# Kernel optimization log

Hardware: AMD Instinct MI355X
Metric: run time of the kernel (lower is better)

Reference implementation:

```python
import jax, jax.numpy as jnp
import numpy as np

B, T, D, DU, H = 2048, 100, 128, 128, 128  # batch, seq_len, emb_dim, user_emb_dim, hidden (=emb_dim)


def _mlp(x, layers, act):
    for W, b in layers:
        x = act(x @ W.T + b)
    return x


def setup_inputs() -> dict:
    key = jax.random.key(0)
    ks = iter(jax.random.split(key, 48))
    def p(shape, scale=0.05):
        return jax.random.normal(next(ks), shape, jnp.float32) * scale
    lengths = jax.random.randint(next(ks), (B,), 1, T + 1).astype(jnp.int32)
    mask = (jnp.arange(T)[None, :] < lengths[:, None]).astype(jnp.int32)
    inp = {
        'user_embedding': p((B, DU), 1.0),
        'item_historical_embedding': p((B, T, D), 1.0),
        'item_embedding': p((B, D), 1.0),
        'mask': mask,
        'sequential_length': lengths,
        'gru_Wih': p((3 * H, D)), 'gru_Whh': p((3 * H, H)),
        'gru_bih': p((3 * H,)), 'gru_bhh': p((3 * H,)),
        'aug_Wr': p((H, D + H)), 'aug_br': p((H,)),
        'aug_Wu': p((H, D + H)), 'aug_bu': p((H,)),
        'aug_Wh': p((H, D + H)), 'aug_bh': p((H,)),
    }
    att_dims = [4 * D, 80, 40, 1]
    ph_dims = [4 * D + DU, 200, 80, 1]
    for i, (di, do) in enumerate(zip(att_dims[:-1], att_dims[1:])):
        inp['att_W%d' % i] = p((do, di)); inp['att_b%d' % i] = p((do,))
    for i, (di, do) in enumerate(zip(ph_dims[:-1], ph_dims[1:])):
        inp['ph_W%d' % i] = p((do, di)); inp['ph_b%d' % i] = p((do,))
    return inp


def _forward(mask, sequential_length, user_embedding, item_historical_embedding, item_embedding,
             gru_Wih, gru_Whh, gru_bih, gru_bhh,
             att_W0, att_b0, att_W1, att_b1, att_W2, att_b2,
             aug_Wr, aug_br, aug_Wu, aug_bu, aug_Wh, aug_bh,
             ph_W0, ph_b0, ph_W1, ph_b1, ph_W2, ph_b2):
    fmask = mask.astype(jnp.float32)
    hist_sum = (item_historical_embedding * fmask[:, :, None]).sum(1)
    hist_sum = hist_sum / sequential_length[:, None].astype(jnp.float32)  # (B, D)

    # standard GRU over time (torch nn.GRU gate math) via lax.scan
    def gru_step(h, x_t):
        gi = x_t @ gru_Wih.T + gru_bih
        gh = h @ gru_Whh.T + gru_bhh
        i_r, i_z, i_n = jnp.split(gi, 3, axis=-1)
        h_r, h_z, h_n = jnp.split(gh, 3, axis=-1)
        r = jax.nn.sigmoid(i_r + h_r)
        z = jax.nn.sigmoid(i_z + h_z)
        n = jnp.tanh(i_n + r * h_n)
        h_new = (1.0 - z) * n + z * h
        return h_new, h_new
    h0 = jnp.zeros((item_historical_embedding.shape[0], H), jnp.float32)
    _, gru_seq = jax.lax.scan(gru_step, h0, jnp.swapaxes(item_historical_embedding, 0, 1))
    keys = jnp.swapaxes(gru_seq, 0, 1)  # (B, T, H)

    # DIN-style activation unit (all-ReLU MLP since act='relu'), masked softmax over time
    q = jnp.broadcast_to(item_embedding[:, None, :], keys.shape)
    feat = jnp.concatenate([keys, q, keys - q, q * keys], axis=-1)  # (B, T, 4H)
    score = _mlp(feat, [(att_W0, att_b0), (att_W1, att_b1), (att_W2, att_b2)], jax.nn.relu)
    score = jnp.where(mask[:, :, None] == 1, score, -jnp.inf)
    attn = jax.nn.softmax(score, axis=1)[..., 0]  # (B, T)
    # return_score=False in source: pooled context vector is (mis)used as attention scores
    pooled = jnp.einsum('bt,btd->bd', attn, keys)  # (B, H)

    # AUGRU; source indexes pooled[:, t] as per-step attention score (requires T <= H)
    att_seq = pooled.T[:T]  # (T, B)
    def augru_step(h, inp):
        x_t, a_t = inp
        ti = jnp.concatenate([h, x_t], axis=-1)
        r = jax.nn.sigmoid(ti @ aug_Wr.T + aug_br)
        u = jax.nn.sigmoid(ti @ aug_Wu.T + aug_bu)
        h_hat = jnp.tanh(jnp.concatenate([h * r, x_t], axis=-1) @ aug_Wh.T + aug_bh)
        u = a_t[:, None] * u
        h_new = (1.0 - u) * h + u * h_hat
        return h_new, h_new
    _, aug_seq = jax.lax.scan(augru_step, h0, (jnp.swapaxes(keys, 0, 1), att_seq))
    aug_out = jnp.swapaxes(aug_seq, 0, 1)  # (B, T, H)

    idx = (sequential_length - 1).astype(jnp.int32)[:, None, None]
    attention_feature = jnp.take_along_axis(aug_out, idx, axis=1)[:, 0, :]  # (B, H)

    comb = jnp.concatenate([user_embedding, item_embedding, hist_sum,
                            item_embedding * hist_sum, attention_feature], axis=1)
    # PredictHead: all layers sigmoid (source's i != len(dims)-1 is always True)
    scores = _mlp(comb, [(ph_W0, ph_b0), (ph_W1, ph_b1), (ph_W2, ph_b2)], jax.nn.sigmoid)
    return scores[:, 0]


def reference(user_embedding, item_historical_embedding, item_embedding, mask, sequential_length,
              gru_Wih, gru_Whh, gru_bih, gru_bhh,
              att_W0, att_b0, att_W1, att_b1, att_W2, att_b2,
              aug_Wr, aug_br, aug_Wu, aug_bu, aug_Wh, aug_bh,
              ph_W0, ph_b0, ph_W1, ph_b1, ph_W2, ph_b2):
    return _forward(mask, sequential_length, user_embedding, item_historical_embedding, item_embedding,
                    gru_Wih, gru_Whh, gru_bih, gru_bhh,
                    att_W0, att_b0, att_W1, att_b1, att_W2, att_b2,
                    aug_Wr, aug_br, aug_Wu, aug_bu, aug_Wh, aug_bh,
                    ph_W0, ph_b0, ph_W1, ph_b1, ph_W2, ph_b2)
```

## Files before the change

kernel.cpp:

```cpp
#include <hip/hip_runtime.h>
#include <math.h>

#define BB 2048
#define TT 100
#define DD 128
#define HH 128

typedef __attribute__((ext_vector_type(8))) short bf16x8;
typedef __attribute__((ext_vector_type(4))) float f32x4;

__device__ __forceinline__ float sigm(float x) {
    return __builtin_amdgcn_rcpf(1.f + __expf(-x));
}
__device__ __forceinline__ float tanh_fast(float x) {
    x = fminf(fmaxf(x, -15.f), 15.f);
    float e = __expf(2.f * x);
    return (e - 1.f) * __builtin_amdgcn_rcpf(e + 1.f);
}
__device__ __forceinline__ short f2bf(float f) {
    union { float f; unsigned u; } v; v.f = f;
    unsigned r = v.u + 0x7FFF + ((v.u >> 16) & 1);
    return (short)(r >> 16);
}
__device__ __forceinline__ float bf2f(ushort u) {
    union { unsigned u; float f; } v; v.u = ((unsigned)u) << 16;
    return v.f;
}

#define RD_A(buf, kk) (*(const bf16x8*)((const char*)(buf) + arow * 256 + (((kk) * 64 + akg * 16) ^ ((arow & 7) << 4))))
#define ST_A(buf, row, c, val) (*(short*)((char*)(buf) + (row) * 256 + (((c) * 2) ^ (((row) & 7) << 4))) = (val))

__global__ void k_prep(const float* __restrict__ attW0,
                       float* __restrict__ Wk, float* __restrict__ Wd, float* __restrict__ WqmC) {
    int i = blockIdx.x * 256 + threadIdx.x;
    if (i < 128 * 80) {
        int d = i / 80, j = i - d * 80;
        Wk[i]   = attW0[j * 512 + d] + attW0[j * 512 + 256 + d];
        Wd[i]   = attW0[j * 512 + 384 + d];
        WqmC[i] = attW0[j * 512 + 128 + d] - attW0[j * 512 + 256 + d];
    }
}

__global__ void k_pack(const float* __restrict__ Wih, const float* __restrict__ Whh,
                       const float* __restrict__ Wr, const float* __restrict__ Wu, const float* __restrict__ Wh,
                       const float* __restrict__ attW1,
                       const float* __restrict__ phW0, const float* __restrict__ phW1,
                       ushort* __restrict__ Pgru, ushort* __restrict__ Pa1, ushort* __restrict__ Pa2,
                       ushort* __restrict__ W1bf, ushort* __restrict__ W0h, ushort* __restrict__ W1h) {
    int n = blockIdx.x * 256 + threadIdx.x;
    if (n < 98304) {
        int tile = n >> 11, kt = (n >> 9) & 3, li = (n >> 3) & 63, e = n & 7;
        int k = kt * 32 + (li >> 4) * 8 + e;
        float s;
        if (tile < 24) { int j = tile * 16 + (li & 15); s = Wih[j * 128 + k]; }
        else           { int j = (tile - 24) * 16 + (li & 15); s = Whh[j * 128 + k]; }
        Pgru[n] = (ushort)f2bf(s);
    }
    if (n < 65536) {
        int tile = n >> 12, kt = (n >> 9) & 7, li = (n >> 3) & 63, e = n & 7;
        int k = kt * 32 + (li >> 4) * 8 + e;
        int jj = tile * 16 + (li & 15);
        float s = (jj < 128) ? Wr[jj * 256 + k] : Wu[(jj - 128) * 256 + k];
        Pa1[n] = (ushort)f2bf(s);
    }
    if (n < 32768) {
        int tile = n >> 12, kt = (n >> 9) & 7, li = (n >> 3) & 63, e = n & 7;
        int k = kt * 32 + (li >> 4) * 8 + e;
        int j = tile * 16 + (li & 15);
        Pa2[n] = (ushort)f2bf(Wh[j * 256 + k]);
    }
    if (n < 4608) {
        int g = n >> 9;
        int nt = g / 3, kt = g - nt * 3;
        int li = (n >> 3) & 63, e = n & 7;
        int k = kt * 32 + (li >> 4) * 8 + e;
        int j2 = nt * 16 + (li & 15);
        float s = (k < 80 && j2 < 40) ? attW1[j2 * 80 + k] : 0.f;
        W1bf[n] = (ushort)f2bf(s);
    }
    if (n < 133120) {
        int g = n >> 9;
        int nt = g / 20, kt = g - nt * 20;
        int li = (n >> 3) & 63, e = n & 7;
        int k = kt * 32 + (li >> 4) * 8 + e;
        int j = nt * 16 + (li & 15);
        W0h[n] = (ushort)f2bf((j < 200) ? phW0[j * 640 + k] : 0.f);
    }
    if (n < 17920) {
        int g = n >> 9;
        int nt = g / 7, kt = g - nt * 7;
        int li = (n >> 3) & 63, e = n & 7;
        int k = kt * 32 + (li >> 4) * 8 + e;
        int j = nt * 16 + (li & 15);
        W1h[n] = (ushort)f2bf((k < 200 && j < 80) ? phW1[j * 200 + k] : 0.f);
    }
}

__global__ void k_weffbf(const float* __restrict__ item, const float* __restrict__ Wk,
                         const float* __restrict__ Wd, const float* __restrict__ WqmC,
                         const float* __restrict__ attb0,
                         ushort* __restrict__ Weffbf, float* __restrict__ bias2) {
    int b = blockIdx.x, tid = threadIdx.x;
    __shared__ float q[128];
    if (tid < 128) q[tid] = item[b * 128 + tid];
    __syncthreads();
    ushort* Wb = Weffbf + (size_t)b * 10240;
    for (int idx = tid; idx < 10240; idx += 256) {
        int e = idx & 7, li = (idx >> 3) & 63, kt = (idx >> 9) & 3, nt = idx >> 11;
        int d = kt * 32 + (li >> 4) * 8 + e;
        int j = nt * 16 + (li & 15);
        Wb[idx] = (ushort)f2bf(Wk[d * 80 + j] + q[d] * Wd[d * 80 + j]);
    }
    if (tid < 80) {
        float s = attb0[tid];
        for (int d = 0; d < 128; ++d) s += q[d] * WqmC[d * 80 + tid];
        bias2[b * 80 + tid] = s;
    }
}

__global__ __launch_bounds__(512) void k_gru_mfma(const float* __restrict__ hist,
                                                  const ushort* __restrict__ Wp,
                                                  const float* __restrict__ bih, const float* __restrict__ bhh,
                                                  const int* __restrict__ len,
                                                  ushort* __restrict__ keysbf, float* __restrict__ hsum) {
    int tid = threadIdx.x;
    int lane = tid & 63, w = tid >> 6;
    int b0 = blockIdx.x * 8;

    __shared__ ushort xbf[16 * 128];
    __shared__ ushort hbf[2][16 * 128];
    __shared__ int    ln_s[8];

    for (int e = tid; e < 16 * 128; e += 512) { xbf[e] = 0; hbf[0][e] = 0; hbf[1][e] = 0; }
    if (tid < 8) ln_s[tid] = len[b0 + tid];

    const bf16x8* Wv = (const bf16x8*)Wp;
    bf16x8 bfx[3][4], bfh[3][4];
#pragma unroll
    for (int g = 0; g < 3; ++g)
#pragma unroll
        for (int kt = 0; kt < 4; ++kt) {
            bfx[g][kt] = Wv[((g * 8 + w) * 4 + kt) * 64 + lane];
            bfh[g][kt] = Wv[(((24 + g * 8 + w)) * 4 + kt) * 64 + lane];
        }

    int arow = lane & 15, akg = lane >> 4;
    int c = w * 16 + arow;
    float birq = bih[c] + bhh[c];
    float bizq = bih[128 + c] + bhh[128 + c];
    float bin  = bih[256 + c];
    float bqn  = bhh[256 + c];
    float hold[4] = {0.f, 0.f, 0.f, 0.f};

    __syncthreads();

    int srow = tid >> 6, sd0 = (tid & 63) * 2;
    int Lrow = ln_s[srow];
    const float* hsrc = &hist[(size_t)(b0 + srow) * TT * DD + sd0];
    float2 v = *(const float2*)hsrc;
    float sum0 = 0.f, sum1 = 0.f;
    int p = 0;

    for (int t = 0; t < TT; ++t) {
        {
            unsigned pv = (unsigned)(unsigned short)f2bf(v.x) | ((unsigned)(unsigned short)f2bf(v.y) << 16);
            *(unsigned*)((char*)xbf + srow * 256 + ((sd0 * 2) ^ ((srow & 7) << 4))) = pv;
            if (t < Lrow) { sum0 += v.x; sum1 += v.y; }
            if (t + 1 < TT) v = *(const float2*)(hsrc + (size_t)(t + 1) * DD);
        }
        __syncthreads();

        const ushort* hb = hbf[p];
        bf16x8 ax[4], ah[4];
#pragma unroll
        for (int kt = 0; kt < 4; ++kt) { ax[kt] = RD_A(xbf, kt); ah[kt] = RD_A(hb, kt); }

        f32x4 accr = {0.f,0.f,0.f,0.f}, accz = {0.f,0.f,0.f,0.f};
        f32x4 accnx = {0.f,0.f,0.f,0.f}, accnh = {0.f,0.f,0.f,0.f};
#pragma unroll
        for (int kt = 0; kt < 4; ++kt) {
            accr  = __builtin_amdgcn_mfma_f32_16x16x32_bf16(ax[kt], bfx[0][kt], accr, 0, 0, 0);
            accr  = __builtin_amdgcn_mfma_f32_16x16x32_bf16(ah[kt], bfh[0][kt], accr, 0, 0, 0);
            accz  = __builtin_amdgcn_mfma_f32_16x16x32_bf16(ax[kt], bfx[1][kt], accz, 0, 0, 0);
            accz  = __builtin_amdgcn_mfma_f32_16x16x32_bf16(ah[kt], bfh[1][kt], accz, 0, 0, 0);
            accnx = __builtin_amdgcn_mfma_f32_16x16x32_bf16(ax[kt], bfx[2][kt], accnx, 0, 0, 0);
            accnh = __builtin_amdgcn_mfma_f32_16x16x32_bf16(ah[kt], bfh[2][kt], accnh, 0, 0, 0);
        }

        ushort* hbw = (ushort*)hbf[p ^ 1];
#pragma unroll
        for (int i = 0; i < 4; ++i) {
            float r = sigm(accr[i] + birq);
            float z = sigm(accz[i] + bizq);
            float nn = tanh_fast(accnx[i] + bin + r * (accnh[i] + bqn));
            float hnew = (1.f - z) * nn + z * hold[i];
            hold[i] = hnew;
            if (akg < 2) {
                int row = akg * 4 + i;
                short hb16 = f2bf(hnew);
                ST_A(hbw, row, c, hb16);
                keysbf[((size_t)(b0 + row) * TT + t) * HH + c] = (ushort)hb16;
            }
        }
        p ^= 1;
        __syncthreads();
    }

    hsum[(b0 + srow) * 128 + sd0]     = sum0 / (float)Lrow;
    hsum[(b0 + srow) * 128 + sd0 + 1] = sum1 / (float)Lrow;
}

__global__ __launch_bounds__(512) void k_attnsoft(const ushort* __restrict__ keysbf,
                                                  const ushort* __restrict__ Weffbf,
                                                  const float* __restrict__ bias2,
                                                  const ushort* __restrict__ W1bf,
                                                  const float* __restrict__ attb1, const float* __restrict__ attW2,
                                                  const float* __restrict__ attb2,
                                                  const int* __restrict__ len,
                                                  float* __restrict__ pooled) {
    int tid = threadIdx.x;
    int lane = tid & 63, w = tid >> 6;
    int b = blockIdx.x;

    __shared__ ushort kbf[112 * 128];
    __shared__ ushort scbf[112 * 96];
    __shared__ float  bias2s[80];
    __shared__ float  b1s[48];
    __shared__ float  W2s[48];
    __shared__ float  attn_s[128];
    __shared__ float  red[128];

    bf16x8 bfrag0[5][4];
    bf16x8 bfrag1[3][3];
    if (w < 7) {
        const bf16x8* Wb = (const bf16x8*)(Weffbf + (size_t)b * 10240);
#pragma unroll
        for (int nt = 0; nt < 5; ++nt)
#pragma unroll
            for (int kt = 0; kt < 4; ++kt)
                bfrag0[nt][kt] = Wb[(nt * 4 + kt) * 64 + lane];
#pragma unroll
        for (int nt = 0; nt < 3; ++nt)
#pragma unroll
            for (int kt = 0; kt < 3; ++kt)
                bfrag1[nt][kt] = ((const bf16x8*)W1bf)[(nt * 3 + kt) * 64 + lane];
    }

    const ushort* ksrc = keysbf + (size_t)b * TT * 128;
    for (int e = tid; e < 3584; e += 512) {
        int row = e >> 5, c4 = e & 31;
        uint2 pv;
        if (row < TT) pv = *(const uint2*)(ksrc + row * 128 + c4 * 4);
        else { pv.x = 0; pv.y = 0; }
        *(uint2*)((char*)kbf + row * 256 + ((c4 * 8) ^ ((row & 7) << 4))) = pv;
    }
    for (int e = tid; e < 1792; e += 512) {
        int row = e >> 4, c = 80 + (e & 15);
        *(ushort*)((char*)scbf + row * 192 + ((c * 2) ^ ((row & 7) << 4))) = 0;
    }
    if (tid < 80) bias2s[tid] = bias2[b * 80 + tid];
    if (tid < 48) {
        b1s[tid] = (tid < 40) ? attb1[tid] : 0.f;
        W2s[tid] = (tid < 40) ? attW2[tid] : 0.f;
    }
    __syncthreads();

    if (w < 7) {
        int arow = lane & 15, akg = lane >> 4;
        int row = w * 16 + arow;
        bf16x8 af[4];
#pragma unroll
        for (int kt = 0; kt < 4; ++kt)
            af[kt] = *(const bf16x8*)((const char*)kbf + row * 256 + (((kt * 64 + akg * 16)) ^ ((row & 7) << 4)));
#pragma unroll
        for (int nt = 0; nt < 5; ++nt) {
            f32x4 acc = {0.f, 0.f, 0.f, 0.f};
#pragma unroll
            for (int kt = 0; kt < 4; ++kt)
                acc = __builtin_amdgcn_mfma_f32_16x16x32_bf16(af[kt], bfrag0[nt][kt], acc, 0, 0, 0);
            int col = nt * 16 + arow;
            float bcol = bias2s[col];
#pragma unroll
            for (int i = 0; i < 4; ++i) {
                int r2 = w * 16 + akg * 4 + i;
                float vsc = fmaxf(acc[i] + bcol, 0.f);
                *(short*)((char*)scbf + r2 * 192 + ((col * 2) ^ ((r2 & 7) << 4))) = f2bf(vsc);
            }
        }
    }
    __syncthreads();

    if (w < 7) {
        int arow = lane & 15, akg = lane >> 4;
        int row = w * 16 + arow;
        bf16x8 a1[3];
#pragma unroll
        for (int kt = 0; kt < 3; ++kt)
            a1[kt] = *(const bf16x8*)((const char*)scbf + row * 192 + (((kt * 64 + akg * 16)) ^ ((row & 7) << 4)));
        float pi[4] = {0.f, 0.f, 0.f, 0.f};
#pragma unroll
        for (int nt = 0; nt < 3; ++nt) {
            f32x4 acc = {0.f, 0.f, 0.f, 0.f};
#pragma unroll
            for (int kt = 0; kt < 3; ++kt)
                acc = __builtin_amdgcn_mfma_f32_16x16x32_bf16(a1[kt], bfrag1[nt][kt], acc, 0, 0, 0);
            int col = nt * 16 + arow;
            float wb = W2s[col], bb1 = b1s[col];
#pragma unroll
            for (int i = 0; i < 4; ++i)
                pi[i] += fmaxf(acc[i] + bb1, 0.f) * wb;
        }
#pragma unroll
        for (int off = 1; off < 16; off <<= 1)
#pragma unroll
            for (int i = 0; i < 4; ++i)
                pi[i] += __shfl_xor(pi[i], off);
        if ((lane & 15) == 0) {
            float b2 = attb2[0];
#pragma unroll
            for (int i = 0; i < 4; ++i) {
                int t = w * 16 + akg * 4 + i;
                if (t < 128) attn_s[t] = fmaxf(pi[i] + b2, 0.f);
            }
        }
    }
    __syncthreads();

    int L = len[b];
    if (tid < 128) red[tid] = (tid < L) ? attn_s[tid] : -INFINITY;
    __syncthreads();
    for (int o = 64; o >= 1; o >>= 1) { if (tid < o) red[tid] = fmaxf(red[tid], red[tid + o]); __syncthreads(); }
    float mx = red[0];
    __syncthreads();
    if (tid < 128) {
        float e = (tid < L) ? __expf(attn_s[tid] - mx) : 0.f;
        attn_s[tid] = e; red[tid] = e;
    }
    __syncthreads();
    for (int o = 64; o >= 1; o >>= 1) { if (tid < o) red[tid] += red[tid + o]; __syncthreads(); }
    float inv = __builtin_amdgcn_rcpf(red[0]);
    if (tid < 128) {
        int d = tid;
        float p = 0.f;
        for (int t2 = 0; t2 < L; ++t2) {
            ushort kv = *(const ushort*)((const char*)kbf + t2 * 256 + ((d * 2) ^ ((t2 & 7) << 4)));
            p += attn_s[t2] * bf2f(kv);
        }
        pooled[b * 128 + d] = p * inv;
    }
}

__global__ __launch_bounds__(512) void k_augru_mfma(const ushort* __restrict__ keysbf,
                                                    const float* __restrict__ pooled,
                                                    const int* __restrict__ len,
                                                    const ushort* __restrict__ Wp1, const ushort* __restrict__ Wp2,
                                                    const float* __restrict__ br, const float* __restrict__ bu,
                                                    const float* __restrict__ bh,
                                                    float* __restrict__ att_feat) {
    int tid = threadIdx.x;
    int lane = tid & 63, w = tid >> 6;
    int b0 = blockIdx.x * 8;

    __shared__ ushort hbf[16 * 128], xbf[16 * 128], rhbf[16 * 128];
    __shared__ float as_[16];
    __shared__ int ln_s[8];

    for (int e = tid; e < 16 * 128; e += 512) { hbf[e] = 0; xbf[e] = 0; rhbf[e] = 0; }
    if (tid < 16) as_[tid] = 0.f;
    if (tid < 8) ln_s[tid] = len[b0 + tid];

    const bf16x8* W1v = (const bf16x8*)Wp1;
    const bf16x8* W2v = (const bf16x8*)Wp2;
    bf16x8 b1r[8], b1u[8], b2[8];
#pragma unroll
    for (int kt = 0; kt < 8; ++kt) {
        b1r[kt] = W1v[(w * 8 + kt) * 64 + lane];
        b1u[kt] = W1v[((8 + w) * 8 + kt) * 64 + lane];
        b2[kt]  = W2v[(w * 8 + kt) * 64 + lane];
    }

    int arow = lane & 15, akg = lane >> 4;
    int c = w * 16 + arow;
    float brc = br[c], buc = bu[c], bhc = bh[c];
    float hold[4] = {0.f, 0.f, 0.f, 0.f};

    int srow = tid >> 6, sd0 = (tid & 63) * 2;
    const ushort* xsrc = &keysbf[(size_t)(b0 + srow) * TT * HH + sd0];
    unsigned v0 = *(const unsigned*)xsrc;
    __syncthreads();
    *(unsigned*)((char*)xbf + srow * 256 + ((sd0 * 2) ^ ((srow & 7) << 4))) = v0;
    unsigned vnext = (TT > 1) ? *(const unsigned*)(xsrc + (size_t)1 * HH) : 0u;
    float areg = 0.f;
    if (tid < 8) {
        as_[tid] = pooled[(b0 + tid) * HH + 0];
        if (TT > 1) areg = pooled[(b0 + tid) * HH + 1];
    }
    __syncthreads();

    for (int t = 0; t < TT; ++t) {
        bf16x8 ah[4], ax[4];
#pragma unroll
        for (int kt = 0; kt < 4; ++kt) { ah[kt] = RD_A(hbf, kt); ax[kt] = RD_A(xbf, kt); }
        f32x4 accr = {0.f,0.f,0.f,0.f}, accu = {0.f,0.f,0.f,0.f};
#pragma unroll
        for (int kt = 0; kt < 4; ++kt) {
            accr = __builtin_amdgcn_mfma_f32_16x16x32_bf16(ah[kt], b1r[kt], accr, 0, 0, 0);
            accr = __builtin_amdgcn_mfma_f32_16x16x32_bf16(ax[kt], b1r[4 + kt], accr, 0, 0, 0);
            accu = __builtin_amdgcn_mfma_f32_16x16x32_bf16(ah[kt], b1u[kt], accu, 0, 0, 0);
            accu = __builtin_amdgcn_mfma_f32_16x16x32_bf16(ax[kt], b1u[4 + kt], accu, 0, 0, 0);
        }
        float u_reg[4];
#pragma unroll
        for (int i = 0; i < 4; ++i) {
            float r = sigm(accr[i] + brc);
            float a = as_[akg * 4 + i];
            u_reg[i] = a * sigm(accu[i] + buc);
            if (akg < 2) ST_A(rhbf, akg * 4 + i, c, f2bf(r * hold[i]));
        }
        __syncthreads();

        bf16x8 arh[4];
#pragma unroll
        for (int kt = 0; kt < 4; ++kt) arh[kt] = RD_A(rhbf, kt);
        f32x4 acch = {0.f,0.f,0.f,0.f};
#pragma unroll
        for (int kt = 0; kt < 4; ++kt) {
            acch = __builtin_amdgcn_mfma_f32_16x16x32_bf16(arh[kt], b2[kt], acch, 0, 0, 0);
            acch = __builtin_amdgcn_mfma_f32_16x16x32_bf16(ax[kt], b2[4 + kt], acch, 0, 0, 0);
        }
#pragma unroll
        for (int i = 0; i < 4; ++i) {
            float hhat = tanh_fast(acch[i] + bhc);
            float hnew = (1.f - u_reg[i]) * hold[i] + u_reg[i] * hhat;
            hold[i] = hnew;
            if (akg < 2) {
                int row = akg * 4 + i;
                ST_A(hbf, row, c, f2bf(hnew));
                if (t == ln_s[row] - 1) att_feat[(b0 + row) * HH + c] = hnew;
            }
        }
        if (t + 1 < TT) {
            *(unsigned*)((char*)xbf + srow * 256 + ((sd0 * 2) ^ ((srow & 7) << 4))) = vnext;
            if (tid < 8) as_[tid] = areg;
            if (t + 2 < TT) {
                vnext = *(const unsigned*)(xsrc + (size_t)(t + 2) * HH);
                if (tid < 8) areg = pooled[(b0 + tid) * HH + t + 2];
            }
        }
        __syncthreads();
    }
}

__global__ __launch_bounds__(64) void k_head(const float* __restrict__ user, const float* __restrict__ item,
                                             const float* __restrict__ hsum, const float* __restrict__ attf,
                                             const ushort* __restrict__ W0h, const ushort* __restrict__ W1h,
                                             const float* __restrict__ phb0, const float* __restrict__ phb1,
                                             const float* __restrict__ phW2, const float* __restrict__ phb2,
                                             float* __restrict__ out) {
    int lane = threadIdx.x;
    int b0 = blockIdx.x * 16;
    __shared__ ushort xb[16 * 128];
    __shared__ ushort h1b[16 * 256];

    for (int e = lane; e < 4096; e += 64) h1b[e] = 0;

    int arow = lane & 15, akg = lane >> 4;
    f32x4 acc0[13];
#pragma unroll
    for (int nt = 0; nt < 13; ++nt) acc0[nt] = (f32x4){0.f, 0.f, 0.f, 0.f};

    for (int c = 0; c < 5; ++c) {
        for (int idx = lane; idx < 1024; idx += 64) {
            int row = idx >> 6, c2 = (idx & 63) * 2;
            int g = (b0 + row) * 128 + c2;
            float2 v;
            if (c == 0) v = *(const float2*)&user[g];
            else if (c == 1) v = *(const float2*)&item[g];
            else if (c == 2) v = *(const float2*)&hsum[g];
            else if (c == 3) { float2 a = *(const float2*)&item[g]; float2 h = *(const float2*)&hsum[g];
                               v.x = a.x * h.x; v.y = a.y * h.y; }
            else v = *(const float2*)&attf[g];
            unsigned pv = (unsigned)(unsigned short)f2bf(v.x) | ((unsigned)(unsigned short)f2bf(v.y) << 16);
            *(unsigned*)((char*)xb + row * 256 + ((c2 * 2) ^ ((row & 7) << 4))) = pv;
        }
        __syncthreads();
        bf16x8 af[4];
#pragma unroll
        for (int kt = 0; kt < 4; ++kt)
            af[kt] = *(const bf16x8*)((const char*)xb + arow * 256 + ((kt * 64 + akg * 16) ^ ((arow & 7) << 4)));
#pragma unroll
        for (int nt = 0; nt < 13; ++nt) {
#pragma unroll
            for (int kt = 0; kt < 4; ++kt) {
                int ktg = c * 4 + kt;
                bf16x8 bf = ((const bf16x8*)W0h)[(nt * 20 + ktg) * 64 + lane];
                acc0[nt] = __builtin_amdgcn_mfma_f32_16x16x32_bf16(af[kt], bf, acc0[nt], 0, 0, 0);
            }
        }
        __syncthreads();
    }

#pragma unroll
    for (int nt = 0; nt < 13; ++nt) {
        int col = nt * 16 + arow;
        if (col < 200) {
            float bb = phb0[col];
#pragma unroll
            for (int i = 0; i < 4; ++i) {
                int r2 = akg * 4 + i;
                *(short*)((char*)h1b + r2 * 512 + ((col * 2) ^ ((r2 & 7) << 4))) = f2bf(sigm(acc0[nt][i] + bb));
            }
        }
    }
    __syncthreads();

    bf16x8 a1[7];
#pragma unroll
    for (int kt = 0; kt < 7; ++kt)
        a1[kt] = *(const bf16x8*)((const char*)h1b + arow * 512 + ((kt * 64 + akg * 16) ^ ((arow & 7) << 4)));
    float pi[4] = {0.f, 0.f, 0.f, 0.f};
#pragma unroll
    for (int nt = 0; nt < 5; ++nt) {
        f32x4 acc = {0.f, 0.f, 0.f, 0.f};
#pragma unroll
        for (int kt = 0; kt < 7; ++kt)
            acc = __builtin_amdgcn_mfma_f32_16x16x32_bf16(a1[kt], ((const bf16x8*)W1h)[(nt * 7 + kt) * 64 + lane], acc, 0, 0, 0);
        int col = nt * 16 + arow;
        float b1 = phb1[col], w2v = phW2[col];
#pragma unroll
        for (int i = 0; i < 4; ++i)
            pi[i] += sigm(acc[i] + b1) * w2v;
    }
#pragma unroll
    for (int off = 1; off < 16; off <<= 1)
#pragma unroll
        for (int i = 0; i < 4; ++i)
            pi[i] += __shfl_xor(pi[i], off);
    if (arow == 0) {
        float b2 = phb2[0];
#pragma unroll
        for (int i = 0; i < 4; ++i)
            out[b0 + akg * 4 + i] = sigm(pi[i] + b2);
    }
}

extern "C" void kernel_launch(void* const* d_in, const int* in_sizes, int n_in,
                              void* d_out, int out_size, void* d_ws, size_t ws_size,
                              hipStream_t stream) {
    const float* user = (const float*)d_in[0];
    const float* hist = (const float*)d_in[1];
    const float* item = (const float*)d_in[2];
    const int* len = (const int*)d_in[4];
    const float* gWih = (const float*)d_in[5];
    const float* gWhh = (const float*)d_in[6];
    const float* gbih = (const float*)d_in[7];
    const float* gbhh = (const float*)d_in[8];
    const float* aWr = (const float*)d_in[9];
    const float* abr = (const float*)d_in[10];
    const float* aWu = (const float*)d_in[11];
    const float* abu = (const float*)d_in[12];
    const float* aWh = (const float*)d_in[13];
    const float* abh = (const float*)d_in[14];
    const float* attW0 = (const float*)d_in[15];
    const float* attb0 = (const float*)d_in[16];
    const float* attW1 = (const float*)d_in[17];
    const float* attb1 = (const float*)d_in[18];
    const float* attW2 = (const float*)d_in[19];
    const float* attb2 = (const float*)d_in[20];
    const float* phW0 = (const float*)d_in[21];
    const float* phb0 = (const float*)d_in[22];
    const float* phW1 = (const float*)d_in[23];
    const float* phb1 = (const float*)d_in[24];
    const float* phW2 = (const float*)d_in[25];
    const float* phb2 = (const float*)d_in[26];

    char* ws = (char*)d_ws;
    size_t off = 0;
    auto alloc = [&](size_t bytes) { char* p = ws + off; off += (bytes + 255) & ~(size_t)255; return p; };
    ushort* keysbf  = (ushort*)alloc((size_t)BB * TT * HH * 2);
    ushort* Weffbf  = (ushort*)alloc((size_t)BB * 10240 * 2);
    float* pooled   = (float*)alloc((size_t)BB * HH * 4);
    float* hsum     = (float*)alloc((size_t)BB * DD * 4);
    float* attf     = (float*)alloc((size_t)BB * HH * 4);
    float* Wk       = (float*)alloc(128 * 80 * 4);
    float* Wd       = (float*)alloc(128 * 80 * 4);
    float* WqmC     = (float*)alloc(128 * 80 * 4);
    float* bias2    = (float*)alloc((size_t)BB * 80 * 4);
    ushort* Pgru    = (ushort*)alloc(98304 * 2);
    ushort* Pa1     = (ushort*)alloc(65536 * 2);
    ushort* Pa2     = (ushort*)alloc(32768 * 2);
    ushort* W1bf    = (ushort*)alloc(4608 * 2);
    ushort* W0h     = (ushort*)alloc(133120 * 2);
    ushort* W1h     = (ushort*)alloc(17920 * 2);
    (void)in_sizes; (void)n_in; (void)out_size; (void)ws_size;

    k_prep<<<40, 256, 0, stream>>>(attW0, Wk, Wd, WqmC);
    k_pack<<<520, 256, 0, stream>>>(gWih, gWhh, aWr, aWu, aWh, attW1, phW0, phW1,
                                    Pgru, Pa1, Pa2, W1bf, W0h, W1h);
    k_weffbf<<<BB, 256, 0, stream>>>(item, Wk, Wd, WqmC, attb0, Weffbf, bias2);
    k_gru_mfma<<<256, 512, 0, stream>>>(hist, Pgru, gbih, gbhh, len, keysbf, hsum);
    k_attnsoft<<<BB, 512, 0, stream>>>(keysbf, Weffbf, bias2, W1bf, attb1, attW2, attb2, len, pooled);
    k_augru_mfma<<<256, 512, 0, stream>>>(keysbf, pooled, len, Pa1, Pa2, abr, abu, abh, attf);
    k_head<<<128, 64, 0, stream>>>(user, item, hsum, attf, W0h, W1h, phb0, phb1, phW2, phb2, (float*)d_out);
}
```

Before: 410.2 us.

## Software-pipeline input projections in GRU/AUGRU recurrences and split attention pooling

In the GRU kernel, the x-projection MFMAs for step t+1 now run after the barrier of step t. They use a double-buffered x tile, so only the h-dependent MFMAs sit on the recurrent critical path and one barrier per step is removed. The AUGRU kernel loads its x fragments straight from global memory into registers, which drops the shared x buffer. It also precomputes the next step's x contributions to the r, u and h gates in the gap between the two phases. Attention pooling now spreads the time loop across all 512 threads with a shared-memory reduction, at the cost of more registers and an extra barrier.

Result: slower. 432.7 us (+5.5%).

```diff
diff --git a/kernel.cpp b/kernel.cpp
--- a/kernel.cpp
+++ b/kernel.cpp
@@ -127,11 +127,11 @@
     int lane = tid & 63, w = tid >> 6;
     int b0 = blockIdx.x * 8;
 
-    __shared__ ushort xbf[16 * 128];
+    __shared__ ushort xbf[2][16 * 128];
     __shared__ ushort hbf[2][16 * 128];
     __shared__ int    ln_s[8];
 
-    for (int e = tid; e < 16 * 128; e += 512) { xbf[e] = 0; hbf[0][e] = 0; hbf[1][e] = 0; }
+    for (int e = tid; e < 16 * 128; e += 512) { xbf[0][e] = 0; xbf[1][e] = 0; hbf[0][e] = 0; hbf[1][e] = 0; }
     if (tid < 8) ln_s[tid] = len[b0 + tid];
 
     const bf16x8* Wv = (const bf16x8*)Wp;
@@ -152,42 +152,55 @@
     float bqn  = bhh[256 + c];
     float hold[4] = {0.f, 0.f, 0.f, 0.f};
 
-    __syncthreads();
-
     int srow = tid >> 6, sd0 = (tid & 63) * 2;
-    int Lrow = ln_s[srow];
     const float* hsrc = &hist[(size_t)(b0 + srow) * TT * DD + sd0];
     float2 v = *(const float2*)hsrc;
+    __syncthreads();
+    int Lrow = ln_s[srow];
     float sum0 = 0.f, sum1 = 0.f;
-    int p = 0;
-
+    {
+        unsigned pv = (unsigned)(unsigned short)f2bf(v.x) | ((unsigned)(unsigned short)f2bf(v.y) << 16);
+        *(unsigned*)((char*)xbf[0] + srow * 256 + ((sd0 * 2) ^ ((srow & 7) << 4))) = pv;
+        if (0 < Lrow) { sum0 += v.x; sum1 += v.y; }
+        if (TT > 1) v = *(const float2*)(hsrc + DD);
+    }
+    __syncthreads();
+
+    f32x4 accr, accz, accnx;
+    {
+        bf16x8 af[4];
+#pragma unroll
+        for (int kt = 0; kt < 4; ++kt) af[kt] = RD_A(xbf[0], kt);
+        accr = (f32x4){0.f,0.f,0.f,0.f}; accz = accr; accnx = accr;
+#pragma unroll
+        for (int kt = 0; kt < 4; ++kt) {
+            accr  = __builtin_amdgcn_mfma_f32_16x16x32_bf16(af[kt], bfx[0][kt], accr, 0, 0, 0);
+            accz  = __builtin_amdgcn_mfma_f32_16x16x32_bf16(af[kt], bfx[1][kt], accz, 0, 0, 0);
+            accnx = __builtin_amdgcn_mfma_f32_16x16x32_bf16(af[kt], bfx[2][kt], accnx, 0, 0, 0);
+        }
+    }
+
+    int p = 0, q = 0;
     for (int t = 0; t < TT; ++t) {
-        {
+        if (t + 1 < TT) {
             unsigned pv = (unsigned)(unsigned short)f2bf(v.x) | ((unsigned)(unsigned short)f2bf(v.y) << 16);
-            *(unsigned*)((char*)xbf + srow * 256 + ((sd0 * 2) ^ ((srow & 7) << 4))) = pv;
-            if (t < Lrow) { sum0 += v.x; sum1 += v.y; }
-            if (t + 1 < TT) v = *(const float2*)(hsrc + (size_t)(t + 1) * DD);
-        }
-        __syncthreads();
-
-        const ushort* hb = hbf[p];
-        bf16x8 ax[4], ah[4];
-#pragma unroll
-        for (int kt = 0; kt < 4; ++kt) { ax[kt] = RD_A(xbf, kt); ah[kt] = RD_A(hb, kt); }
-
-        f32x4 accr = {0.f,0.f,0.f,0.f}, accz = {0.f,0.f,0.f,0.f};
-        f32x4 accnx = {0.f,0.f,0.f,0.f}, accnh = {0.f,0.f,0.f,0.f};
+            *(unsigned*)((char*)xbf[p ^ 1] + srow * 256 + ((sd0 * 2) ^ ((srow & 7) << 4))) = pv;
+            if (t + 1 < Lrow) { sum0 += v.x; sum1 += v.y; }
+            if (t + 2 < TT) v = *(const float2*)(hsrc + (size_t)(t + 2) * DD);
+        }
+
+        bf16x8 ah[4];
+#pragma unroll
+        for (int kt = 0; kt < 4; ++kt) ah[kt] = RD_A(hbf[q], kt);
+        f32x4 accnh = {0.f, 0.f, 0.f, 0.f};
 #pragma unroll
         for (int kt = 0; kt < 4; ++kt) {
-            accr  = __builtin_amdgcn_mfma_f32_16x16x32_bf16(ax[kt], bfx[0][kt], accr, 0, 0, 0);
             accr  = __builtin_amdgcn_mfma_f32_16x16x32_bf16(ah[kt], bfh[0][kt], accr, 0, 0, 0);
-            accz  = __builtin_amdgcn_mfma_f32_16x16x32_bf16(ax[kt], bfx[1][kt], accz, 0, 0, 0);
             accz  = __builtin_amdgcn_mfma_f32_16x16x32_bf16(ah[kt], bfh[1][kt], accz, 0, 0, 0);
-            accnx = __builtin_amdgcn_mfma_f32_16x16x32_bf16(ax[kt], bfx[2][kt], accnx, 0, 0, 0);
             accnh = __builtin_amdgcn_mfma_f32_16x16x32_bf16(ah[kt], bfh[2][kt], accnh, 0, 0, 0);
         }
 
-        ushort* hbw = (ushort*)hbf[p ^ 1];
+        ushort* hw = (ushort*)hbf[q ^ 1];
 #pragma unroll
         for (int i = 0; i < 4; ++i) {
             float r = sigm(accr[i] + birq);
@@ -198,12 +211,26 @@
             if (akg < 2) {
                 int row = akg * 4 + i;
                 short hb16 = f2bf(hnew);
-                ST_A(hbw, row, c, hb16);
+                ST_A(hw, row, c, hb16);
                 keysbf[((size_t)(b0 + row) * TT + t) * HH + c] = (ushort)hb16;
             }
         }
-        p ^= 1;
         __syncthreads();
+
+        if (t + 1 < TT) {
+            bf16x8 af[4];
+#pragma unroll
+            for (int kt = 0; kt < 4; ++kt) af[kt] = RD_A(xbf[p ^ 1], kt);
+            f32x4 ar = {0.f,0.f,0.f,0.f}, az = ar, an = ar;
+#pragma unroll
+            for (int kt = 0; kt < 4; ++kt) {
+                ar = __builtin_amdgcn_mfma_f32_16x16x32_bf16(af[kt], bfx[0][kt], ar, 0, 0, 0);
+                az = __builtin_amdgcn_mfma_f32_16x16x32_bf16(af[kt], bfx[1][kt], az, 0, 0, 0);
+                an = __builtin_amdgcn_mfma_f32_16x16x32_bf16(af[kt], bfx[2][kt], an, 0, 0, 0);
+            }
+            accr = ar; accz = az; accnx = an;
+        }
+        p ^= 1; q ^= 1;
     }
 
     hsum[(b0 + srow) * 128 + sd0]     = sum0 / (float)Lrow;
@@ -229,6 +256,7 @@
     __shared__ float  W2s[48];
     __shared__ float  attn_s[128];
     __shared__ float  red[128];
+    __shared__ float  pred[512];
 
     bf16x8 bfrag0[5][4];
     bf16x8 bfrag1[3][3];
@@ -339,15 +367,18 @@
     __syncthreads();
     for (int o = 64; o >= 1; o >>= 1) { if (tid < o) red[tid] += red[tid + o]; __syncthreads(); }
     float inv = __builtin_amdgcn_rcpf(red[0]);
-    if (tid < 128) {
-        int d = tid;
+    {
+        int d = tid & 127, qd = tid >> 7;
         float p = 0.f;
-        for (int t2 = 0; t2 < L; ++t2) {
+        for (int t2 = qd; t2 < L; t2 += 4) {
             ushort kv = *(const ushort*)((const char*)kbf + t2 * 256 + ((d * 2) ^ ((t2 & 7) << 4)));
             p += attn_s[t2] * bf2f(kv);
         }
-        pooled[b * 128 + d] = p * inv;
-    }
+        pred[tid] = p;
+    }
+    __syncthreads();
+    if (tid < 128)
+        pooled[b * 128 + tid] = (pred[tid] + pred[128 + tid] + pred[256 + tid] + pred[384 + tid]) * inv;
 }
 
 __global__ __launch_bounds__(512) void k_augru_mfma(const ushort* __restrict__ keysbf,
@@ -361,11 +392,11 @@
     int lane = tid & 63, w = tid >> 6;
     int b0 = blockIdx.x * 8;
 
-    __shared__ ushort hbf[16 * 128], xbf[16 * 128], rhbf[16 * 128];
+    __shared__ ushort hbf[16 * 128], rhbf[16 * 128];
     __shared__ float as_[16];
     __shared__ int ln_s[8];
 
-    for (int e = tid; e < 16 * 128; e += 512) { hbf[e] = 0; xbf[e] = 0; rhbf[e] = 0; }
+    for (int e = tid; e < 16 * 128; e += 512) { hbf[e] = 0; rhbf[e] = 0; }
     if (tid < 16) as_[tid] = 0.f;
     if (tid < 8) ln_s[tid] = len[b0 + tid];
 
@@ -384,37 +415,46 @@
     float brc = br[c], buc = bu[c], bhc = bh[c];
     float hold[4] = {0.f, 0.f, 0.f, 0.f};
 
-    int srow = tid >> 6, sd0 = (tid & 63) * 2;
-    const ushort* xsrc = &keysbf[(size_t)(b0 + srow) * TT * HH + sd0];
-    unsigned v0 = *(const unsigned*)xsrc;
-    __syncthreads();
-    *(unsigned*)((char*)xbf + srow * 256 + ((sd0 * 2) ^ ((srow & 7) << 4))) = v0;
-    unsigned vnext = (TT > 1) ? *(const unsigned*)(xsrc + (size_t)1 * HH) : 0u;
-    float areg = 0.f;
-    if (tid < 8) {
-        as_[tid] = pooled[(b0 + tid) * HH + 0];
-        if (TT > 1) areg = pooled[(b0 + tid) * HH + 1];
-    }
-    __syncthreads();
+    int rowg = b0 + arow; if (rowg > BB - 1) rowg = BB - 1;
+    const ushort* xbase = keysbf + (size_t)rowg * TT * HH + akg * 8;
+
+    bf16x8 axc[4], axn[4];
+#pragma unroll
+    for (int kt = 0; kt < 4; ++kt) axc[kt] = *(const bf16x8*)(xbase + kt * 32);
+    float areg = (tid < 8) ? pooled[(b0 + tid) * HH + 0] : 0.f;
+    if (tid < 8) as_[tid] = areg;
+    float aregn = (tid < 8 && TT > 1) ? pooled[(b0 + tid) * HH + 1] : 0.f;
+    __syncthreads();
+
+    f32x4 accr = {0.f,0.f,0.f,0.f}, accu = {0.f,0.f,0.f,0.f};
+#pragma unroll
+    for (int kt = 0; kt < 4; ++kt) {
+        accr = __builtin_amdgcn_mfma_f32_16x16x32_bf16(axc[kt], b1r[4 + kt], accr, 0, 0, 0);
+        accu = __builtin_amdgcn_mfma_f32_16x16x32_bf16(axc[kt], b1u[4 + kt], accu, 0, 0, 0);
+    }
 
     for (int t = 0; t < TT; ++t) {
-        bf16x8 ah[4], ax[4];
-#pragma unroll
-        for (int kt = 0; kt < 4; ++kt) { ah[kt] = RD_A(hbf, kt); ax[kt] = RD_A(xbf, kt); }
-        f32x4 accr = {0.f,0.f,0.f,0.f}, accu = {0.f,0.f,0.f,0.f};
+        if (t + 1 < TT) {
+#pragma unroll
+            for (int kt = 0; kt < 4; ++kt) axn[kt] = *(const bf16x8*)(xbase + (size_t)(t + 1) * HH + kt * 32);
+        }
+
+        bf16x8 ah[4];
+#pragma unroll
+        for (int kt = 0; kt < 4; ++kt) ah[kt] = RD_A(hbf, kt);
+        f32x4 acch = {0.f,0.f,0.f,0.f};
 #pragma unroll
         for (int kt = 0; kt < 4; ++kt) {
             accr = __builtin_amdgcn_mfma_f32_16x16x32_bf16(ah[kt], b1r[kt], accr, 0, 0, 0);
-            accr = __builtin_amdgcn_mfma_f32_16x16x32_bf16(ax[kt], b1r[4 + kt], accr, 0, 0, 0);
             accu = __builtin_amdgcn_mfma_f32_16x16x32_bf16(ah[kt], b1u[kt], accu, 0, 0, 0);
-            accu = __builtin_amdgcn_mfma_f32_16x16x32_bf16(ax[kt], b1u[4 + kt], accu, 0, 0, 0);
-        }
+            acch = __builtin_amdgcn_mfma_f32_16x16x32_bf16(axc[kt], b2[4 + kt], acch, 0, 0, 0);
+        }
+
         float u_reg[4];
 #pragma unroll
         for (int i = 0; i < 4; ++i) {
             float r = sigm(accr[i] + brc);
-            float a = as_[akg * 4 + i];
-            u_reg[i] = a * sigm(accu[i] + buc);
+            u_reg[i] = as_[akg * 4 + i] * sigm(accu[i] + buc);
             if (akg < 2) ST_A(rhbf, akg * 4 + i, c, f2bf(r * hold[i]));
         }
         __syncthreads();
@@ -422,12 +462,14 @@
         bf16x8 arh[4];
 #pragma unroll
         for (int kt = 0; kt < 4; ++kt) arh[kt] = RD_A(rhbf, kt);
-        f32x4 acch = {0.f,0.f,0.f,0.f};
+        f32x4 accr2 = {0.f,0.f,0.f,0.f}, accu2 = {0.f,0.f,0.f,0.f};
 #pragma unroll
         for (int kt = 0; kt < 4; ++kt) {
             acch = __builtin_amdgcn_mfma_f32_16x16x32_bf16(arh[kt], b2[kt], acch, 0, 0, 0);
-            acch = __builtin_amdgcn_mfma_f32_16x16x32_bf16(ax[kt], b2[4 + kt], acch, 0, 0, 0);
-        }
+            accr2 = __builtin_amdgcn_mfma_f32_16x16x32_bf16(axn[kt], b1r[4 + kt], accr2, 0, 0, 0);
+            accu2 = __builtin_amdgcn_mfma_f32_16x16x32_bf16(axn[kt], b1u[4 + kt], accu2, 0, 0, 0);
+        }
+
 #pragma unroll
         for (int i = 0; i < 4; ++i) {
             float hhat = tanh_fast(acch[i] + bhc);
@@ -439,15 +481,13 @@
                 if (t == ln_s[row] - 1) att_feat[(b0 + row) * HH + c] = hnew;
             }
         }
-        if (t + 1 < TT) {
-            *(unsigned*)((char*)xbf + srow * 256 + ((sd0 * 2) ^ ((srow & 7) << 4))) = vnext;
-            if (tid < 8) as_[tid] = areg;
-            if (t + 2 < TT) {
-                vnext = *(const unsigned*)(xsrc + (size_t)(t + 2) * HH);
-                if (tid < 8) areg = pooled[(b0 + tid) * HH + t + 2];
-            }
-        }
+        if (tid < 8) as_[tid] = aregn;
+        if (tid < 8 && t + 2 < TT) aregn = pooled[(b0 + tid) * HH + t + 2];
         __syncthreads();
+
+        accr = accr2; accu = accu2;
+#pragma unroll
+        for (int kt = 0; kt < 4; ++kt) axc[kt] = axn[kt];
     }
 }
 
```
